# Performance work log

Hardware: AMD Instinct MI355X
Metric: run time of the kernel (lower is better)

## Reference

```python
import jax, jax.numpy as jnp
import numpy as np

POINTS_PER_UNIT = 64
EPS = 1e-8


def setup_inputs() -> dict:
    key = jax.random.key(0)
    k1, k2 = jax.random.split(key)
    b, n, c, m = 4, 1024, 16, 1024
    # context inputs in [-2, 2]
    xz = jax.random.uniform(k1, (b, n, 1), dtype=jnp.float32, minval=-2.0, maxval=2.0)
    z = jax.random.normal(k2, (b, n, c), dtype=jnp.float32)
    # uniform grid covering the data range with a small margin (stands in for discretisation(xz, x))
    x_grid = jnp.linspace(-2.1, 2.1, m, dtype=jnp.float32)
    # learnable length-scale, init = log(2 / points_per_unit)
    log_scale = jnp.full((1,), np.log(2.0 / POINTS_PER_UNIT), dtype=jnp.float32)
    return {"xz": xz, "z": z, "x_grid": x_grid, "log_scale": log_scale}


def reference(xz, z, x_grid, log_scale):
    b, n, c = z.shape
    m = x_grid.shape[0]
    # pairwise squared distances between context locations and grid: [b, n, m]
    dists2 = (xz[:, :, 0:1] - x_grid[None, None, :]) ** 2
    # Gaussian (RBF) kernel weights
    weights = jnp.exp(-0.5 * dists2 / jnp.exp(2.0 * log_scale[0]))  # [b, n, m]
    # prepend density channel of ones: [b, n, c+1]
    zc = jnp.concatenate([jnp.ones((b, n, 1), z.dtype), z], axis=2)
    # out[b,k,i,j] = sum_n weights[b,n,i] * zc[b,n,k] * weights[b,n,j]
    # (matches B.matmul(weights * z, weights, tr_a=True) in the original)
    out = jnp.einsum('bni,bnk,bnj->bkij', weights, zc, weights)  # [b, c+1, m, m]
    density = out[:, :1]
    # KDE normalization of data channels by the density channel
    out = jnp.concatenate([density, out[:, 1:] / (density + EPS)], axis=1)
    # prepend identity channel: [b, 1, m, m]
    identity = jnp.broadcast_to(jnp.eye(m, dtype=z.dtype), (b, 1, m, m))
    out = jnp.concatenate([identity, out], axis=1)  # [b, c+2, m, m]
    return (x_grid, out)
```

## Files before the change

### kernel.cpp

```cpp
#include <hip/hip_runtime.h>

typedef float v2f __attribute__((ext_vector_type(2)));
typedef float v4f __attribute__((ext_vector_type(4)));

#define NPTS  1024
#define MGRID 1024
#define NCH   16
#define MAXL  256

__global__ __launch_bounds__(256, 4)
void setconv_kernel(const float* __restrict__ xz,
                    const float* __restrict__ z,
                    const float* __restrict__ x_grid,
                    const float* __restrict__ log_scale,
                    float* __restrict__ out)
{
    const int bx   = blockIdx.x;
    const int b    = blockIdx.y;
    const int tid  = threadIdx.x;
    const int w    = tid >> 6;
    const int lane = tid & 63;
    const int i0   = bx * 4;
    const int i    = i0 + w;

    __shared__ float xz_l[MAXL];
    __shared__ v4f   z_l[MAXL * 4];
    __shared__ int   cnts[4];

    const float s2   = __expf(2.0f * log_scale[0]);
    const float cexp = -0.5f / s2;
    const float r8   = 8.0f * __expf(log_scale[0]);
    const float h    = x_grid[1] - x_grid[0];
    const float gi0  = x_grid[i0];
    const float gi   = x_grid[i];
    const float lo   = gi0 - r8;
    const float hi   = gi0 + 3.0f * h + r8;

    int jb = i0 - 128;
    jb = jb < 0 ? 0 : (jb > MGRID - 256 ? MGRID - 256 : jb);
    const float gj0 = x_grid[jb + 4 * lane];

    const float* xzb = xz + b * NPTS;
    float xv[4]; unsigned long long msk[4]; int idx[4];
    int base = 0;
    #pragma unroll
    for (int r = 0; r < 4; ++r) {
        const int n = 256 * w + 64 * r + lane;
        xv[r] = xzb[n];
        const bool pred = (xv[r] > lo) && (xv[r] < hi);
        msk[r] = __ballot(pred);
        idx[r] = base + (int)__popcll(msk[r] & ((1ull << lane) - 1ull));
        base += (int)__popcll(msk[r]);
    }
    if (lane == 0) cnts[w] = base;
    __syncthreads();

    int off = 0, total = 0;
    #pragma unroll
    for (int s = 0; s < 4; ++s) { const int c = cnts[s]; if (s < w) off += c; total += c; }
    if (total > MAXL) total = MAXL;

    const v4f* zb4 = (const v4f*)(z + (size_t)b * NPTS * NCH);
    #pragma unroll
    for (int r = 0; r < 4; ++r) {
        if ((msk[r] >> lane) & 1ull) {
            const int slot = off + idx[r];
            if (slot < MAXL) {
                const int n = 256 * w + 64 * r + lane;
                xz_l[slot] = xv[r];
                #pragma unroll
                for (int q = 0; q < 4; ++q)
                    z_l[slot * 4 + q] = zb4[n * 4 + q];
            }
        }
    }
    __syncthreads();

    float* big = out + MGRID;
    const size_t plane = (size_t)MGRID * MGRID;
    float* rb = big + (size_t)b * 18 * plane + (size_t)i * MGRID;
    const int wstart = jb >> 2;

    const float tc  = -2.0f * cexp * h;
    const float ch2 = cexp * h * h;
    const float K1  = __expf(ch2);
    const float K2  = __expf(4.0f * ch2);
    const float K3  = __expf(9.0f * ch2);

    v2f   num2[4][8];
    float den[4] = {0.f, 0.f, 0.f, 0.f};
    #pragma unroll
    for (int jj = 0; jj < 4; ++jj)
        #pragma unroll
        for (int k = 0; k < 8; ++k) num2[jj][k] = (v2f){0.f, 0.f};

    const v4f zero4 = {0.f, 0.f, 0.f, 0.f};

    for (int t = 0; t < total; ++t) {
        if (t < 18) {
            if (t == 0) {
                v4f* rp = (v4f*)rb;
                #pragma unroll
                for (int it = 0; it < 4; ++it) {
                    const int q  = it * 64 + lane;
                    const int j0 = q * 4;
                    v4f v;
                    v.x = (j0 + 0 == i) ? 1.f : 0.f;
                    v.y = (j0 + 1 == i) ? 1.f : 0.f;
                    v.z = (j0 + 2 == i) ? 1.f : 0.f;
                    v.w = (j0 + 3 == i) ? 1.f : 0.f;
                    __builtin_nontemporal_store(v, rp + q);
                }
                if (b == 0 && bx < 4)
                    out[bx * 256 + tid] = x_grid[bx * 256 + tid];
            } else {
                v4f* rp = (v4f*)(rb + (size_t)t * plane);
                #pragma unroll
                for (int it = 0; it < 3; ++it) {
                    const int q = it * 64 + lane;
                    const int f = (q < wstart) ? q : q + 64;
                    __builtin_nontemporal_store(zero4, rp + f);
                }
            }
        }

        const float xzn = xz_l[t];
        const v4f a0 = z_l[t * 4 + 0], a1 = z_l[t * 4 + 1],
                  a2 = z_l[t * 4 + 2], a3 = z_l[t * 4 + 3];
        const float d0 = xzn - gj0;
        const float di = xzn - gi;
        const float E  = __expf(cexp * (d0 * d0 + di * di));
        const float T  = __expf(tc * d0);
        const float T2 = T * T;

        float p[4];
        p[0] = E;
        p[1] = E * K1 * T;
        p[2] = E * K2 * T2;
        p[3] = E * K3 * (T2 * T);

        const v2f za[8] = {{a0.x, a0.y}, {a0.z, a0.w}, {a1.x, a1.y}, {a1.z, a1.w},
                           {a2.x, a2.y}, {a2.z, a2.w}, {a3.x, a3.y}, {a3.z, a3.w}};
        #pragma unroll
        for (int jj = 0; jj < 4; ++jj) {
            den[jj] += p[jj];
            const v2f pp = {p[jj], p[jj]};
            #pragma unroll
            for (int k = 0; k < 8; ++k)
                num2[jj][k] = pp * za[k] + num2[jj][k];
        }
    }

    float rcp[4];
    #pragma unroll
    for (int jj = 0; jj < 4; ++jj) rcp[jj] = 1.0f / (den[jj] + 1e-8f);

    const int fw = wstart + lane;

    {
        const v4f dv = {den[0], den[1], den[2], den[3]};
        __builtin_nontemporal_store(dv, (v4f*)(rb + plane) + fw);
    }
    #pragma unroll
    for (int k = 0; k < NCH; ++k) {
        const int k2 = k >> 1, lsel = k & 1;
        const v4f rv = {num2[0][k2][lsel] * rcp[0], num2[1][k2][lsel] * rcp[1],
                        num2[2][k2][lsel] * rcp[2], num2[3][k2][lsel] * rcp[3]};
        __builtin_nontemporal_store(rv, (v4f*)(rb + (size_t)(2 + k) * plane) + fw);
    }
}

extern "C" void kernel_launch(void* const* d_in, const int* in_sizes, int n_in,
                              void* d_out, int out_size, void* d_ws, size_t ws_size,
                              hipStream_t stream)
{
    const float* xz = (const float*)d_in[0];
    const float* z  = (const float*)d_in[1];
    const float* xg = (const float*)d_in[2];
    const float* ls = (const float*)d_in[3];
    float* out = (float*)d_out;

    setconv_kernel<<<dim3(MGRID / 4, 4), dim3(256), 0, stream>>>(xz, z, xg, ls, out);
}
```

Before: 337.4 us.

## Split identity and zero-band fill into a separate kernel before compute

Moves the identity-plane and off-band zero writes out of the compute kernel's accumulation loop into a dedicated fill kernel launched over every (row-block, channel, batch). The compute kernel now writes only the banded density and normalized channels, and those stores become ordinary stores instead of nontemporal ones. The aim is to take the store work out of the hot loop and to stop it depending on the per-block count of context points. The cost is an extra launch and running the fill and the compute serially, with no overlap between them.

```diff
diff --git a/kernel.cpp b/kernel.cpp
--- a/kernel.cpp
+++ b/kernel.cpp
@@ -7,6 +7,50 @@
 #define MGRID 1024
 #define NCH   16
 #define MAXL  256
+
+__global__ __launch_bounds__(256)
+void fill_kernel(float* __restrict__ out)
+{
+    const int bx   = blockIdx.x;
+    const int ch   = blockIdx.y;
+    const int b    = blockIdx.z;
+    const int tid  = threadIdx.x;
+    const int w    = tid >> 6;
+    const int lane = tid & 63;
+    const int i0   = bx * 4;
+
+    int jb = i0 - 128;
+    jb = jb < 0 ? 0 : (jb > MGRID - 256 ? MGRID - 256 : jb);
+    const int wstart = jb >> 2;
+
+    float* big = out + MGRID;
+    const size_t plane = (size_t)MGRID * MGRID;
+    v4f* rp = (v4f*)(big + (size_t)b * 18 * plane + (size_t)ch * plane
+                         + (size_t)(i0 + w) * MGRID);
+
+    if (ch == 0) {
+        const int i = i0 + w;
+        #pragma unroll
+        for (int it = 0; it < 4; ++it) {
+            const int q  = it * 64 + lane;
+            const int j0 = q * 4;
+            v4f v;
+            v.x = (j0 + 0 == i) ? 1.f : 0.f;
+            v.y = (j0 + 1 == i) ? 1.f : 0.f;
+            v.z = (j0 + 2 == i) ? 1.f : 0.f;
+            v.w = (j0 + 3 == i) ? 1.f : 0.f;
+            rp[q] = v;
+        }
+    } else {
+        const v4f zero4 = {0.f, 0.f, 0.f, 0.f};
+        #pragma unroll
+        for (int it = 0; it < 3; ++it) {
+            const int q = it * 64 + lane;
+            const int f = (q < wstart) ? q : q + 64;
+            rp[f] = zero4;
+        }
+    }
+}
 
 __global__ __launch_bounds__(256, 4)
 void setconv_kernel(const float* __restrict__ xz,
@@ -40,6 +84,9 @@
     jb = jb < 0 ? 0 : (jb > MGRID - 256 ? MGRID - 256 : jb);
     const float gj0 = x_grid[jb + 4 * lane];
 
+    if (b == 0 && bx < 4)
+        out[bx * 256 + tid] = x_grid[bx * 256 + tid];
+
     const float* xzb = xz + b * NPTS;
     float xv[4]; unsigned long long msk[4]; int idx[4];
     int base = 0;
@@ -94,36 +141,7 @@
         #pragma unroll
         for (int k = 0; k < 8; ++k) num2[jj][k] = (v2f){0.f, 0.f};
 
-    const v4f zero4 = {0.f, 0.f, 0.f, 0.f};
-
     for (int t = 0; t < total; ++t) {
-        if (t < 18) {
-            if (t == 0) {
-                v4f* rp = (v4f*)rb;
-                #pragma unroll
-                for (int it = 0; it < 4; ++it) {
-                    const int q  = it * 64 + lane;
-                    const int j0 = q * 4;
-                    v4f v;
-                    v.x = (j0 + 0 == i) ? 1.f : 0.f;
-                    v.y = (j0 + 1 == i) ? 1.f : 0.f;
-                    v.z = (j0 + 2 == i) ? 1.f : 0.f;
-                    v.w = (j0 + 3 == i) ? 1.f : 0.f;
-                    __builtin_nontemporal_store(v, rp + q);
-                }
-                if (b == 0 && bx < 4)
-                    out[bx * 256 + tid] = x_grid[bx * 256 + tid];
-            } else {
-                v4f* rp = (v4f*)(rb + (size_t)t * plane);
-                #pragma unroll
-                for (int it = 0; it < 3; ++it) {
-                    const int q = it * 64 + lane;
-                    const int f = (q < wstart) ? q : q + 64;
-                    __builtin_nontemporal_store(zero4, rp + f);
-                }
-            }
-        }
-
         const float xzn = xz_l[t];
         const v4f a0 = z_l[t * 4 + 0], a1 = z_l[t * 4 + 1],
                   a2 = z_l[t * 4 + 2], a3 = z_l[t * 4 + 3];
@@ -159,14 +177,14 @@
 
     {
         const v4f dv = {den[0], den[1], den[2], den[3]};
-        __builtin_nontemporal_store(dv, (v4f*)(rb + plane) + fw);
+        ((v4f*)(rb + plane))[fw] = dv;
     }
     #pragma unroll
     for (int k = 0; k < NCH; ++k) {
         const int k2 = k >> 1, lsel = k & 1;
         const v4f rv = {num2[0][k2][lsel] * rcp[0], num2[1][k2][lsel] * rcp[1],
                         num2[2][k2][lsel] * rcp[2], num2[3][k2][lsel] * rcp[3]};
-        __builtin_nontemporal_store(rv, (v4f*)(rb + (size_t)(2 + k) * plane) + fw);
+        ((v4f*)(rb + (size_t)(2 + k) * plane))[fw] = rv;
     }
 }
 
@@ -180,5 +198,7 @@
     const float* ls = (const float*)d_in[3];
     float* out = (float*)d_out;
 
+    fill_kernel<<<dim3(MGRID / 4, 18, 4), dim3(256), 0, stream>>>(out);
+
     setconv_kernel<<<dim3(MGRID / 4, 4), dim3(256), 0, stream>>>(xz, z, xg, ls, out);
 }
```

After: 380.2 us. +12.7%, slower.

## Move identity/zero fill into separate linear fill kernel before compute

Applied to the files above, without the earlier changes.

Adds a separate fill kernel that writes the identity plane and zeros every other plane with fully linear, coalesced stores. The interleaved scattered zero stores are removed from the compute loop. The compute kernel now overwrites only the band window, using ordinary rather than nontemporal stores. The trade is a second launch and a full extra write of the banded region, about 72 MB in total instead of only the off-band parts, in exchange for better store coalescing and a leaner inner loop.

```diff
diff --git a/kernel.cpp b/kernel.cpp
--- a/kernel.cpp
+++ b/kernel.cpp
@@ -7,6 +7,37 @@
 #define MGRID 1024
 #define NCH   16
 #define MAXL  256
+
+__global__ __launch_bounds__(256)
+void fill_linear(float* __restrict__ out)
+{
+    const int bid = blockIdx.x;
+    const int tid = threadIdx.x;
+    const int p   = bid >> 6;
+    const int ch  = p % 18;
+    v4f* rp = (v4f*)(out + MGRID) + (size_t)bid * 4096;
+
+    if (ch != 0) {
+        const v4f z4 = {0.f, 0.f, 0.f, 0.f};
+        #pragma unroll
+        for (int it = 0; it < 16; ++it)
+            rp[it * 256 + tid] = z4;
+    } else {
+        const int row0 = (bid & 63) * 16;
+        #pragma unroll
+        for (int it = 0; it < 16; ++it) {
+            const int F   = it * 256 + tid;
+            const int row = row0 + (F >> 8);
+            const int j0  = (F & 255) << 2;
+            v4f v;
+            v.x = (j0 + 0 == row) ? 1.f : 0.f;
+            v.y = (j0 + 1 == row) ? 1.f : 0.f;
+            v.z = (j0 + 2 == row) ? 1.f : 0.f;
+            v.w = (j0 + 3 == row) ? 1.f : 0.f;
+            rp[F] = v;
+        }
+    }
+}
 
 __global__ __launch_bounds__(256, 4)
 void setconv_kernel(const float* __restrict__ xz,
@@ -39,6 +70,9 @@
     int jb = i0 - 128;
     jb = jb < 0 ? 0 : (jb > MGRID - 256 ? MGRID - 256 : jb);
     const float gj0 = x_grid[jb + 4 * lane];
+
+    if (b == 0 && bx < 4)
+        out[bx * 256 + tid] = x_grid[bx * 256 + tid];
 
     const float* xzb = xz + b * NPTS;
     float xv[4]; unsigned long long msk[4]; int idx[4];
@@ -94,36 +128,7 @@
         #pragma unroll
         for (int k = 0; k < 8; ++k) num2[jj][k] = (v2f){0.f, 0.f};
 
-    const v4f zero4 = {0.f, 0.f, 0.f, 0.f};
-
     for (int t = 0; t < total; ++t) {
-        if (t < 18) {
-            if (t == 0) {
-                v4f* rp = (v4f*)rb;
-                #pragma unroll
-                for (int it = 0; it < 4; ++it) {
-                    const int q  = it * 64 + lane;
-                    const int j0 = q * 4;
-                    v4f v;
-                    v.x = (j0 + 0 == i) ? 1.f : 0.f;
-                    v.y = (j0 + 1 == i) ? 1.f : 0.f;
-                    v.z = (j0 + 2 == i) ? 1.f : 0.f;
-                    v.w = (j0 + 3 == i) ? 1.f : 0.f;
-                    __builtin_nontemporal_store(v, rp + q);
-                }
-                if (b == 0 && bx < 4)
-                    out[bx * 256 + tid] = x_grid[bx * 256 + tid];
-            } else {
-                v4f* rp = (v4f*)(rb + (size_t)t * plane);
-                #pragma unroll
-                for (int it = 0; it < 3; ++it) {
-                    const int q = it * 64 + lane;
-                    const int f = (q < wstart) ? q : q + 64;
-                    __builtin_nontemporal_store(zero4, rp + f);
-                }
-            }
-        }
-
         const float xzn = xz_l[t];
         const v4f a0 = z_l[t * 4 + 0], a1 = z_l[t * 4 + 1],
                   a2 = z_l[t * 4 + 2], a3 = z_l[t * 4 + 3];
@@ -159,14 +164,14 @@
 
     {
         const v4f dv = {den[0], den[1], den[2], den[3]};
-        __builtin_nontemporal_store(dv, (v4f*)(rb + plane) + fw);
+        ((v4f*)(rb + plane))[fw] = dv;
     }
     #pragma unroll
     for (int k = 0; k < NCH; ++k) {
         const int k2 = k >> 1, lsel = k & 1;
         const v4f rv = {num2[0][k2][lsel] * rcp[0], num2[1][k2][lsel] * rcp[1],
                         num2[2][k2][lsel] * rcp[2], num2[3][k2][lsel] * rcp[3]};
-        __builtin_nontemporal_store(rv, (v4f*)(rb + (size_t)(2 + k) * plane) + fw);
+        ((v4f*)(rb + (size_t)(2 + k) * plane))[fw] = rv;
     }
 }
 
@@ -180,5 +185,7 @@
     const float* ls = (const float*)d_in[3];
     float* out = (float*)d_out;
 
+    fill_linear<<<dim3(72 * 64), dim3(256), 0, stream>>>(out);
+
     setconv_kernel<<<dim3(MGRID / 4, 4), dim3(256), 0, stream>>>(xz, z, xg, ls, out);
 }
```

Measured after the change: 385.0 us. 14.1% more time.

## Factor Gaussian product into midpoint table and separable emit pass

Applied to the files above, without the earlier changes.

Splits the kernel into two passes. The first builds a per-batch table of Gaussian-weighted channel sums at half-grid midpoints, and the second writes each output element as a difference-dependent Gaussian factor times a table lookup. This replaces the per-pair accumulation over context points with a 1D table computation, so the remaining cost is mostly the output writes. It adds a workspace buffer, a second launch, extra reads from the table, and full-plane computation instead of zeros outside the cutoff band.

```diff
diff --git a/kernel.cpp b/kernel.cpp
--- a/kernel.cpp
+++ b/kernel.cpp
@@ -1,44 +1,41 @@
 #include <hip/hip_runtime.h>
 
-typedef float v2f __attribute__((ext_vector_type(2)));
 typedef float v4f __attribute__((ext_vector_type(4)));
 
-#define NPTS  1024
-#define MGRID 1024
-#define NCH   16
-#define MAXL  256
+#define NPTS    1024
+#define MGRID   1024
+#define NCH     16
+#define MAXL    320
+#define UPB     8
+#define FSTRIDE 2048
+#define CUT     0.32f
 
-__global__ __launch_bounds__(256, 4)
-void setconv_kernel(const float* __restrict__ xz,
+
+__global__ __launch_bounds__(256)
+void f_table_kernel(const float* __restrict__ xz,
                     const float* __restrict__ z,
                     const float* __restrict__ x_grid,
                     const float* __restrict__ log_scale,
-                    float* __restrict__ out)
+                    float* __restrict__ F)
 {
-    const int bx   = blockIdx.x;
+    const int ug   = blockIdx.x;
     const int b    = blockIdx.y;
     const int tid  = threadIdx.x;
     const int w    = tid >> 6;
     const int lane = tid & 63;
-    const int i0   = bx * 4;
-    const int i    = i0 + w;
+    const int u0   = ug * UPB;
 
     __shared__ float xz_l[MAXL];
     __shared__ v4f   z_l[MAXL * 4];
     __shared__ int   cnts[4];
 
     const float s2   = __expf(2.0f * log_scale[0]);
-    const float cexp = -0.5f / s2;
-    const float r8   = 8.0f * __expf(log_scale[0]);
-    const float h    = x_grid[1] - x_grid[0];
-    const float gi0  = x_grid[i0];
-    const float gi   = x_grid[i];
-    const float lo   = gi0 - r8;
-    const float hi   = gi0 + 3.0f * h + r8;
+    const float ninv = -1.0f / s2;
 
-    int jb = i0 - 128;
-    jb = jb < 0 ? 0 : (jb > MGRID - 256 ? MGRID - 256 : jb);
-    const float gj0 = x_grid[jb + 4 * lane];
+    const int  u7  = (u0 + UPB - 1) > 2046 ? 2046 : (u0 + UPB - 1);
+    const float m_lo = 0.5f * (x_grid[u0 >> 1] + x_grid[u0 - (u0 >> 1)]);
+    const float m_hi = 0.5f * (x_grid[u7 >> 1] + x_grid[u7 - (u7 >> 1)]);
+    const float lo = m_lo - CUT, hi = m_hi + CUT;
 
     const float* xzb = xz + b * NPTS;
     float xv[4]; unsigned long long msk[4]; int idx[4];
@@ -76,98 +73,83 @@
     }
     __syncthreads();
 
+    const int ul = tid >> 5;
+    const int kk = tid & 31;
+    const int u  = u0 + ul;
+    const int uu = u > 2046 ? 2046 : u;
+    const float xm = 0.5f * (x_grid[uu >> 1] + x_grid[uu - (uu >> 1)]);
+
+    const float* zl = (const float*)z_l;
+    const int zidx0 = (kk == 0) ? 0 : (kk - 1);
+    const bool isone = (kk == 0);
+
+    float acc = 0.0f;
+    for (int t = 0; t < total; ++t) {
+        const float d = xz_l[t] - xm;
+        const float e = __expf(ninv * (d * d));
+        const float val = isone ? 1.0f : zl[t * 16 + zidx0];
+        acc += e * val;
+    }
+
+    if (kk < 17 && u <= 2046)
+        F[((b * 17 + kk) << 11) + u] = acc;
+}
+
+__global__ __launch_bounds__(256)
+void emit_kernel(const float* __restrict__ x_grid,
+                 const float* __restrict__ log_scale,
+                 const float* __restrict__ F,
+                 float* __restrict__ out)
+{
+    const int i  = blockIdx.x;
+    const int b  = blockIdx.y;
+    const int t  = threadIdx.x;
+    const int j0 = t * 4;
+
+    const float s2 = __expf(2.0f * log_scale[0]);
+    const float h  = x_grid[1] - x_grid[0];
+    const float cB = -(h * h) / (4.0f * s2);
+
+    const float* Fb = F + (b * 17) * FSTRIDE;
+
+    float B[4], den[4], inv[4];
+    #pragma unroll
+    for (int l = 0; l < 4; ++l) {
+        const int dj = i - (j0 + l);
+        B[l]   = __expf(cB * (float)(dj * dj));
+        den[l] = B[l] * Fb[i + j0 + l];
+        inv[l] = 1.0f / (den[l] + 1e-8f);
+    }
+
     float* big = out + MGRID;
     const size_t plane = (size_t)MGRID * MGRID;
-    float* rb = big + (size_t)b * 18 * plane + (size_t)i * MGRID;
-    const int wstart = jb >> 2;
+    float* rb = big + ((size_t)b * 18) * plane + (size_t)i * MGRID;
 
-    const float tc  = -2.0f * cexp * h;
-    const float ch2 = cexp * h * h;
-    const float K1  = __expf(ch2);
-    const float K2  = __expf(4.0f * ch2);
-    const float K3  = __expf(9.0f * ch2);
-
-    v2f   num2[4][8];
-    float den[4] = {0.f, 0.f, 0.f, 0.f};
+    {
+        v4f v;
+        v.x = (j0 + 0 == i) ? 1.f : 0.f;
+        v.y = (j0 + 1 == i) ? 1.f : 0.f;
+        v.z = (j0 + 2 == i) ? 1.f : 0.f;
+        v.w = (j0 + 3 == i) ? 1.f : 0.f;
+        ((v4f*)rb)[t] = v;
+    }
+    {
+        const v4f dv = {den[0], den[1], den[2], den[3]};
+        ((v4f*)(rb + plane))[t] = dv;
+    }
     #pragma unroll
-    for (int jj = 0; jj < 4; ++jj)
-        #pragma unroll
-        for (int k = 0; k < 8; ++k) num2[jj][k] = (v2f){0.f, 0.f};
-
-    const v4f zero4 = {0.f, 0.f, 0.f, 0.f};
-
-    for (int t = 0; t < total; ++t) {
-        if (t < 18) {
-            if (t == 0) {
-                v4f* rp = (v4f*)rb;
-                #pragma unroll
-                for (int it = 0; it < 4; ++it) {
-                    const int q  = it * 64 + lane;
-                    const int j0 = q * 4;
-                    v4f v;
-                    v.x = (j0 + 0 == i) ? 1.f : 0.f;
-                    v.y = (j0 + 1 == i) ? 1.f : 0.f;
-                    v.z = (j0 + 2 == i) ? 1.f : 0.f;
-                    v.w = (j0 + 3 == i) ? 1.f : 0.f;
-                    __builtin_nontemporal_store(v, rp + q);
-                }
-                if (b == 0 && bx < 4)
-                    out[bx * 256 + tid] = x_grid[bx * 256 + tid];
-            } else {
-                v4f* rp = (v4f*)(rb + (size_t)t * plane);
-                #pragma unroll
-                for (int it = 0; it < 3; ++it) {
-                    const int q = it * 64 + lane;
-                    const int f = (q < wstart) ? q : q + 64;
-                    __builtin_nontemporal_store(zero4, rp + f);
-                }
-            }
-        }
-
-        const float xzn = xz_l[t];
-        const v4f a0 = z_l[t * 4 + 0], a1 = z_l[t * 4 + 1],
-                  a2 = z_l[t * 4 + 2], a3 = z_l[t * 4 + 3];
-        const float d0 = xzn - gj0;
-        const float di = xzn - gi;
-        const float E  = __expf(cexp * (d0 * d0 + di * di));
-        const float T  = __expf(tc * d0);
-        const float T2 = T * T;
-
-        float p[4];
-        p[0] = E;
-        p[1] = E * K1 * T;
-        p[2] = E * K2 * T2;
-        p[3] = E * K3 * (T2 * T);
-
-        const v2f za[8] = {{a0.x, a0.y}, {a0.z, a0.w}, {a1.x, a1.y}, {a1.z, a1.w},
-                           {a2.x, a2.y}, {a2.z, a2.w}, {a3.x, a3.y}, {a3.z, a3.w}};
-        #pragma unroll
-        for (int jj = 0; jj < 4; ++jj) {
-            den[jj] += p[jj];
-            const v2f pp = {p[jj], p[jj]};
-            #pragma unroll
-            for (int k = 0; k < 8; ++k)
-                num2[jj][k] = pp * za[k] + num2[jj][k];
-        }
+    for (int k = 1; k <= 16; ++k) {
+        const float* Fk = Fb + k * FSTRIDE + i + j0;
+        v4f rv;
+        rv.x = B[0] * Fk[0] * inv[0];
+        rv.y = B[1] * Fk[1] * inv[1];
+        rv.z = B[2] * Fk[2] * inv[2];
+        rv.w = B[3] * Fk[3] * inv[3];
+        ((v4f*)(rb + (size_t)(k + 1) * plane))[t] = rv;
     }
 
-    float rcp[4];
-    #pragma unroll
-    for (int jj = 0; jj < 4; ++jj) rcp[jj] = 1.0f / (den[jj] + 1e-8f);
-
-    const int fw = wstart + lane;
-
-    {
-        const v4f dv = {den[0], den[1], den[2], den[3]};
-        __builtin_nontemporal_store(dv, (v4f*)(rb + plane) + fw);
-    }
-    #pragma unroll
-    for (int k = 0; k < NCH; ++k) {
-        const int k2 = k >> 1, lsel = k & 1;
-        const v4f rv = {num2[0][k2][lsel] * rcp[0], num2[1][k2][lsel] * rcp[1],
-                        num2[2][k2][lsel] * rcp[2], num2[3][k2][lsel] * rcp[3]};
-        __builtin_nontemporal_store(rv, (v4f*)(rb + (size_t)(2 + k) * plane) + fw);
-    }
+    if (b == 0 && i == 0)
+        ((v4f*)out)[t] = ((const v4f*)x_grid)[t];
 }
 
 extern "C" void kernel_launch(void* const* d_in, const int* in_sizes, int n_in,
@@ -179,6 +161,8 @@
     const float* xg = (const float*)d_in[2];
     const float* ls = (const float*)d_in[3];
     float* out = (float*)d_out;
+    float* F   = (float*)d_ws;
 
-    setconv_kernel<<<dim3(MGRID / 4, 4), dim3(256), 0, stream>>>(xz, z, xg, ls, out);
+    f_table_kernel<<<dim3(2048 / UPB, 4), dim3(256), 0, stream>>>(xz, z, xg, ls, F);
+    emit_kernel  <<<dim3(MGRID, 4),      dim3(256), 0, stream>>>(xg, ls, F, out);
 }
```

After: 323.0 us. 4.2% less time.
